# Kernel optimization log

Measured on AMD Instinct MI355X. Metric: run time of the kernel, lower is better.

Reference implementation:

```python
import jax, jax.numpy as jnp
import numpy as np

B, T, DIN, DOUT, RANK = 4, 1, 4096, 11008, 512


def setup_inputs() -> dict:
    key = jax.random.key(0)
    ks = jax.random.split(key, 7)
    inp = jax.random.normal(ks[0], (B, T, DIN), jnp.float32)
    weight = jax.random.normal(ks[1], (DOUT, DIN), jnp.float32) * (1.0 / np.sqrt(DIN))
    bias = jax.random.normal(ks[2], (DOUT,), jnp.float32) * 0.02
    U = jax.random.normal(ks[3], (DOUT, RANK), jnp.float32) * (1.0 / np.sqrt(RANK))
    S = jax.random.uniform(ks[4], (RANK,), jnp.float32, 0.1, 1.0)
    V = jax.random.normal(ks[5], (DIN, RANK), jnp.float32) * (1.0 / np.sqrt(DIN))
    scale = jax.random.uniform(ks[6], (DIN,), jnp.float32, 0.5, 1.5)
    threshold = jnp.full((1,), 0.674, jnp.float32)
    return {"input": inp, "weight": weight, "bias": bias, "U": U, "S": S,
            "V": V, "scale": scale, "threshold": threshold}


def reference(input, weight, bias, U, S, V, scale, threshold):
    # r_sparse mode, decoding path (num_tokens == 1)
    th = threshold[0]
    # mask from scaled magnitudes; piecewise-constant w.r.t. inputs
    s_mask = jax.lax.stop_gradient(
        (jnp.abs(input * scale[None, None, :]) > th).astype(input.dtype))
    # sparse GEMM on masked input: [B,T,DIN] x [DOUT,DIN]^T + bias
    sparse_out = jnp.einsum('btd,od->bto', input * s_mask, weight) + bias
    # low-rank compensation on the complement: x @ (V diag(S)) @ U^T
    lr = jnp.einsum('btd,dr->btr', input * (1.0 - s_mask), V * S[None, :])
    lr = jnp.einsum('btr,or->bto', lr, U)
    return sparse_out + lr
```

## Files before the change

### kernel.cpp

```cpp
#include <hip/hip_runtime.h>
#include <cmath>

constexpr int DIN  = 4096;
constexpr int DOUT = 11008;
constexpr int RANK = 512;
constexpr int NB   = 4;

constexpr int NCHUNK = 256;
constexpr int DCH    = DIN / NCHUNK;

__global__ __launch_bounds__(512)
void lr_partial_kernel(const float* __restrict__ x,
                       const float* __restrict__ scale,
                       const float* __restrict__ thp,
                       const float* __restrict__ V,
                       float* __restrict__ partial,
                       float* __restrict__ xs)
{
    __shared__ float xc[NB * DCH];
    const int chunk = blockIdx.x;
    const int t = threadIdx.x;
    const float th = thp[0];
    if (t < NB * DCH) {
        const int b = t / DCH, dd = t % DCH;
        const int d = chunk * DCH + dd;
        const float xv = x[b * DIN + d];
        const bool keep = fabsf(xv * scale[d]) > th;
        xc[t] = keep ? 0.f : xv;
        xs[b * DIN + d] = keep ? xv : 0.f;
    }
    __syncthreads();
    const int r = t;
    float a0 = 0.f, a1 = 0.f, a2 = 0.f, a3 = 0.f;
    #pragma unroll
    for (int dd = 0; dd < DCH; ++dd) {
        const float v = V[(size_t)(chunk * DCH + dd) * RANK + r];
        a0 = fmaf(xc[0 * DCH + dd], v, a0);
        a1 = fmaf(xc[1 * DCH + dd], v, a1);
        a2 = fmaf(xc[2 * DCH + dd], v, a2);
        a3 = fmaf(xc[3 * DCH + dd], v, a3);
    }
    float* p = partial + (size_t)chunk * (NB * RANK) + r;
    p[0 * RANK] = a0;
    p[1 * RANK] = a1;
    p[2 * RANK] = a2;
    p[3 * RANK] = a3;
}

__global__ __launch_bounds__(64)
void lr_reduce_kernel(const float* __restrict__ partial,
                      const float* __restrict__ S,
                      float* __restrict__ lr)
{
    const int idx = blockIdx.x * 64 + threadIdx.x;
    const int r = idx & (RANK - 1);
    float s = 0.f;
    #pragma unroll 8
    for (int c = 0; c < NCHUNK; ++c)
        s += partial[(size_t)c * (NB * RANK) + idx];
    lr[idx] = s * S[r];
}

__global__ __launch_bounds__(256)
void rsparse_main_kernel(const float* __restrict__ xs,
                         const float* __restrict__ W,
                         const float* __restrict__ bias,
                         const float* __restrict__ U,
                         const float* __restrict__ lr,
                         float* __restrict__ out)
{
    const int tid  = threadIdx.x;
    const int wave = tid >> 6, lane = tid & 63;
    const int o0 = blockIdx.x * 8 + wave * 2;
    const int o1 = o0 + 1;

    const float4* __restrict__ W0 = (const float4*)(W + (size_t)o0 * DIN);
    const float4* __restrict__ W1 = (const float4*)(W + (size_t)o1 * DIN);
    const float4* __restrict__ XS = (const float4*)xs;
    const float4* __restrict__ U0 = (const float4*)(U + (size_t)o0 * RANK);
    const float4* __restrict__ U1 = (const float4*)(U + (size_t)o1 * RANK);
    const float4* __restrict__ LR = (const float4*)lr;

    float acc0[NB] = {0.f, 0.f, 0.f, 0.f};
    float acc1[NB] = {0.f, 0.f, 0.f, 0.f};

    #pragma unroll 4
    for (int k = 0; k < 16; ++k) {
        const int c = (k << 6) + lane;
        const float4 w0 = W0[c];
        const float4 w1 = W1[c];
        #pragma unroll
        for (int b = 0; b < NB; ++b) {
            const float4 xv = XS[b * 1024 + c];
            acc0[b] = fmaf(w0.x, xv.x, acc0[b]);
            acc0[b] = fmaf(w0.y, xv.y, acc0[b]);
            acc0[b] = fmaf(w0.z, xv.z, acc0[b]);
            acc0[b] = fmaf(w0.w, xv.w, acc0[b]);
            acc1[b] = fmaf(w1.x, xv.x, acc1[b]);
            acc1[b] = fmaf(w1.y, xv.y, acc1[b]);
            acc1[b] = fmaf(w1.z, xv.z, acc1[b]);
            acc1[b] = fmaf(w1.w, xv.w, acc1[b]);
        }
    }

    #pragma unroll
    for (int j = 0; j < 2; ++j) {
        const int c = (j << 6) + lane;
        const float4 u0 = U0[c];
        const float4 u1 = U1[c];
        #pragma unroll
        for (int b = 0; b < NB; ++b) {
            const float4 lv = LR[b * 128 + c];
            acc0[b] = fmaf(u0.x, lv.x, acc0[b]);
            acc0[b] = fmaf(u0.y, lv.y, acc0[b]);
            acc0[b] = fmaf(u0.z, lv.z, acc0[b]);
            acc0[b] = fmaf(u0.w, lv.w, acc0[b]);
            acc1[b] = fmaf(u1.x, lv.x, acc1[b]);
            acc1[b] = fmaf(u1.y, lv.y, acc1[b]);
            acc1[b] = fmaf(u1.z, lv.z, acc1[b]);
            acc1[b] = fmaf(u1.w, lv.w, acc1[b]);
        }
    }

    #pragma unroll
    for (int b = 0; b < NB; ++b) {
        #pragma unroll
        for (int m = 32; m >= 1; m >>= 1) {
            acc0[b] += __shfl_xor(acc0[b], m, 64);
            acc1[b] += __shfl_xor(acc1[b], m, 64);
        }
    }

    if (lane == 0) {
        const float bi0 = bias[o0], bi1 = bias[o1];
        #pragma unroll
        for (int b = 0; b < NB; ++b) {
            out[b * DOUT + o0] = acc0[b] + bi0;
            out[b * DOUT + o1] = acc1[b] + bi1;
        }
    }
}

extern "C" void kernel_launch(void* const* d_in, const int* in_sizes, int n_in,
                              void* d_out, int out_size, void* d_ws, size_t ws_size,
                              hipStream_t stream)
{
    const float* x     = (const float*)d_in[0];
    const float* W     = (const float*)d_in[1];
    const float* bias  = (const float*)d_in[2];
    const float* U     = (const float*)d_in[3];
    const float* S     = (const float*)d_in[4];
    const float* V     = (const float*)d_in[5];
    const float* scale = (const float*)d_in[6];
    const float* thp   = (const float*)d_in[7];
    float* out = (float*)d_out;

    float* partial = (float*)d_ws;
    float* lr      = partial + (size_t)NCHUNK * NB * RANK;
    float* xs      = lr + NB * RANK;

    lr_partial_kernel<<<NCHUNK, 512, 0, stream>>>(x, scale, thp, V, partial, xs);
    lr_reduce_kernel<<<(NB * RANK) / 64, 64, 0, stream>>>(partial, S, lr);
    rsparse_main_kernel<<<DOUT / 8, 256, 0, stream>>>(xs, W, bias, U, lr, out);
}
```

Before: 57.31 us.

## Split-K the main GEMV across wave pairs and parallelize LR reduction

The main kernel now splits the DIN reduction across two waves per output pair and writes two partial result buffers. A new final kernel sums them with the bias. The LR reduce kernel spreads each output across 16 threads and combines them with shuffles, instead of one thread doing a serial 256-step loop. Together these raise parallelism and memory-level concurrency, at the cost of an extra launch and an extra partial-buffer round trip through memory.

```diff
diff --git a/kernel.cpp b/kernel.cpp
--- a/kernel.cpp
+++ b/kernel.cpp
@@ -8,6 +8,7 @@
 
 constexpr int NCHUNK = 256;
 constexpr int DCH    = DIN / NCHUNK;
+constexpr int SPLITK = 2;
 
 __global__ __launch_bounds__(512)
 void lr_partial_kernel(const float* __restrict__ x,
@@ -47,46 +48,49 @@
     p[3 * RANK] = a3;
 }
 
-__global__ __launch_bounds__(64)
+__global__ __launch_bounds__(256)
 void lr_reduce_kernel(const float* __restrict__ partial,
                       const float* __restrict__ S,
                       float* __restrict__ lr)
 {
-    const int idx = blockIdx.x * 64 + threadIdx.x;
-    const int r = idx & (RANK - 1);
-    float s = 0.f;
-    #pragma unroll 8
-    for (int c = 0; c < NCHUNK; ++c)
-        s += partial[(size_t)c * (NB * RANK) + idx];
-    lr[idx] = s * S[r];
+    const int t = blockIdx.x * 256 + threadIdx.x;
+    const int idx = t >> 4;
+    const int s = t & 15;
+    float sum = 0.f;
+    #pragma unroll
+    for (int j = 0; j < 16; ++j)
+        sum += partial[(size_t)(s * 16 + j) * (NB * RANK) + idx];
+    #pragma unroll
+    for (int m = 8; m >= 1; m >>= 1)
+        sum += __shfl_xor(sum, m, 64);
+    if (s == 0)
+        lr[idx] = sum * S[idx & (RANK - 1)];
 }
 
 __global__ __launch_bounds__(256)
 void rsparse_main_kernel(const float* __restrict__ xs,
                          const float* __restrict__ W,
-                         const float* __restrict__ bias,
                          const float* __restrict__ U,
                          const float* __restrict__ lr,
-                         float* __restrict__ out)
+                         float* __restrict__ part)
 {
     const int tid  = threadIdx.x;
     const int wave = tid >> 6, lane = tid & 63;
-    const int o0 = blockIdx.x * 8 + wave * 2;
-    const int o1 = o0 + 1;
+    const int pair = blockIdx.x * 2 + (wave >> 1);
+    const int kh   = wave & 1;
+    const int o0 = pair * 2, o1 = o0 + 1;
+    const int kbase = kh * (DIN / SPLITK / 4);
 
     const float4* __restrict__ W0 = (const float4*)(W + (size_t)o0 * DIN);
     const float4* __restrict__ W1 = (const float4*)(W + (size_t)o1 * DIN);
     const float4* __restrict__ XS = (const float4*)xs;
-    const float4* __restrict__ U0 = (const float4*)(U + (size_t)o0 * RANK);
-    const float4* __restrict__ U1 = (const float4*)(U + (size_t)o1 * RANK);
-    const float4* __restrict__ LR = (const float4*)lr;
 
     float acc0[NB] = {0.f, 0.f, 0.f, 0.f};
     float acc1[NB] = {0.f, 0.f, 0.f, 0.f};
 
     #pragma unroll 4
-    for (int k = 0; k < 16; ++k) {
-        const int c = (k << 6) + lane;
+    for (int k = 0; k < 8; ++k) {
+        const int c = kbase + (k << 6) + lane;
         const float4 w0 = W0[c];
         const float4 w1 = W1[c];
         #pragma unroll
@@ -103,22 +107,27 @@
         }
     }
 
-    #pragma unroll
-    for (int j = 0; j < 2; ++j) {
-        const int c = (j << 6) + lane;
-        const float4 u0 = U0[c];
-        const float4 u1 = U1[c];
+    if (kh == 0) {
+        const float4* __restrict__ U0 = (const float4*)(U + (size_t)o0 * RANK);
+        const float4* __restrict__ U1 = (const float4*)(U + (size_t)o1 * RANK);
+        const float4* __restrict__ LR = (const float4*)lr;
         #pragma unroll
-        for (int b = 0; b < NB; ++b) {
-            const float4 lv = LR[b * 128 + c];
-            acc0[b] = fmaf(u0.x, lv.x, acc0[b]);
-            acc0[b] = fmaf(u0.y, lv.y, acc0[b]);
-            acc0[b] = fmaf(u0.z, lv.z, acc0[b]);
-            acc0[b] = fmaf(u0.w, lv.w, acc0[b]);
-            acc1[b] = fmaf(u1.x, lv.x, acc1[b]);
-            acc1[b] = fmaf(u1.y, lv.y, acc1[b]);
-            acc1[b] = fmaf(u1.z, lv.z, acc1[b]);
-            acc1[b] = fmaf(u1.w, lv.w, acc1[b]);
+        for (int j = 0; j < 2; ++j) {
+            const int c = (j << 6) + lane;
+            const float4 u0 = U0[c];
+            const float4 u1 = U1[c];
+            #pragma unroll
+            for (int b = 0; b < NB; ++b) {
+                const float4 lv = LR[b * 128 + c];
+                acc0[b] = fmaf(u0.x, lv.x, acc0[b]);
+                acc0[b] = fmaf(u0.y, lv.y, acc0[b]);
+                acc0[b] = fmaf(u0.z, lv.z, acc0[b]);
+                acc0[b] = fmaf(u0.w, lv.w, acc0[b]);
+                acc1[b] = fmaf(u1.x, lv.x, acc1[b]);
+                acc1[b] = fmaf(u1.y, lv.y, acc1[b]);
+                acc1[b] = fmaf(u1.z, lv.z, acc1[b]);
+                acc1[b] = fmaf(u1.w, lv.w, acc1[b]);
+            }
         }
     }
 
@@ -132,13 +141,23 @@
     }
 
     if (lane == 0) {
-        const float bi0 = bias[o0], bi1 = bias[o1];
+        float* p = part + (size_t)kh * (NB * DOUT);
         #pragma unroll
         for (int b = 0; b < NB; ++b) {
-            out[b * DOUT + o0] = acc0[b] + bi0;
-            out[b * DOUT + o1] = acc1[b] + bi1;
+            p[b * DOUT + o0] = acc0[b];
+            p[b * DOUT + o1] = acc1[b];
         }
     }
+}
+
+__global__ __launch_bounds__(256)
+void final_add_kernel(const float* __restrict__ part,
+                      const float* __restrict__ bias,
+                      float* __restrict__ out)
+{
+    const int i = blockIdx.x * 256 + threadIdx.x;
+    const int o = i % DOUT;
+    out[i] = part[i] + part[NB * DOUT + i] + bias[o];
 }
 
 extern "C" void kernel_launch(void* const* d_in, const int* in_sizes, int n_in,
@@ -158,8 +177,10 @@
     float* partial = (float*)d_ws;
     float* lr      = partial + (size_t)NCHUNK * NB * RANK;
     float* xs      = lr + NB * RANK;
+    float* part    = xs + NB * DIN;
 
     lr_partial_kernel<<<NCHUNK, 512, 0, stream>>>(x, scale, thp, V, partial, xs);
-    lr_reduce_kernel<<<(NB * RANK) / 64, 64, 0, stream>>>(partial, S, lr);
-    rsparse_main_kernel<<<DOUT / 8, 256, 0, stream>>>(xs, W, bias, U, lr, out);
+    lr_reduce_kernel<<<(NB * RANK * 16) / 256, 256, 0, stream>>>(partial, S, lr);
+    rsparse_main_kernel<<<DOUT / 4, 256, 0, stream>>>(xs, W, U, lr, part);
+    final_add_kernel<<<(NB * DOUT) / 256, 256, 0, stream>>>(part, bias, out);
 }
```

New measurement: 52.72 us. -8.0%, faster.
